# Kernel optimization log

Measured on AMD Instinct MI355X. Metric: run time of the kernel, lower is better.

Reference implementation:

```python
import jax, jax.numpy as jnp
import numpy as np

N = 100000      # nodes
E = 1000000     # edges (before self loops)
F_IN = 128      # num_features
G = 512         # graphs in batch
NC = 10         # num_classes
EPS_BN = 1e-5
NEG_SLOPE = 0.2


def setup_inputs() -> dict:
    key = jax.random.key(0)
    ks = iter(jax.random.split(key, 40))
    rn = lambda shape, s=0.1: jax.random.normal(next(ks), shape, jnp.float32) * s
    inp = {
        "x": jax.random.normal(next(ks), (N, F_IN), jnp.float32),
        "edge_index": jax.random.randint(next(ks), (2, E), 0, N),
        "batch": jnp.sort(jax.random.randint(next(ks), (N,), 0, G)),
        "W1": rn((F_IN, 128)), "as1": rn((8, 16)), "ad1": rn((8, 16)), "b1": jnp.zeros((128,), jnp.float32),
        "g1": jnp.ones((128,), jnp.float32), "be1": jnp.zeros((128,), jnp.float32),
        "Wl1": rn((128, 16)), "bl1": jnp.zeros((16,), jnp.float32),
        "gl1": jnp.ones((16,), jnp.float32), "bel1": jnp.zeros((16,), jnp.float32),
        "W2": rn((16, 96)), "as2": rn((4, 24)), "ad2": rn((4, 24)), "b2": jnp.zeros((96,), jnp.float32),
        "g2": jnp.ones((96,), jnp.float32), "be2": jnp.zeros((96,), jnp.float32),
        "Wl2": rn((96, 24)), "bl2": jnp.zeros((24,), jnp.float32),
        "gl2": jnp.ones((24,), jnp.float32), "bel2": jnp.zeros((24,), jnp.float32),
        "W3": rn((24, 64)), "as3": rn((2, 32)), "ad3": rn((2, 32)), "b3": jnp.zeros((64,), jnp.float32),
        "g3": jnp.ones((64,), jnp.float32), "be3": jnp.zeros((64,), jnp.float32),
        # final classifier
        "Wo": rn((64, NC)), "bo": jnp.zeros((NC,), jnp.float32),
    }
    return inp


def _bn(h, gamma, beta):
    # training-mode BatchNorm1d: batch statistics, biased variance
    m = jnp.mean(h, axis=0)
    v = jnp.var(h, axis=0)
    return gamma * (h - m) * jax.lax.rsqrt(v + EPS_BN) + beta


def _gat(h_in, src, dst, W, a_src, a_dst, bias, n):
    heads, ch = a_src.shape
    h = (h_in @ W).reshape(n, heads, ch)                     # [N,H,C]
    alpha_s = jnp.sum(h * a_src, axis=-1)                    # [N,H]
    alpha_d = jnp.sum(h * a_dst, axis=-1)                    # [N,H]
    e = jax.nn.leaky_relu(alpha_s[src] + alpha_d[dst], NEG_SLOPE)   # [E,H]
    emax = jax.ops.segment_max(e, dst, num_segments=n)       # segment softmax over target
    e = jnp.exp(e - emax[dst])
    denom = jax.ops.segment_sum(e, dst, num_segments=n)
    alpha = e / (denom[dst] + 1e-16)                         # [E,H]
    msg = h[src] * alpha[:, :, None]                         # [E,H,C]
    out = jax.ops.segment_sum(msg, dst, num_segments=n)      # [N,H,C]
    return out.reshape(n, heads * ch) + bias


def reference(x, edge_index, batch,
              W1, as1, ad1, b1, g1, be1, Wl1, bl1, gl1, bel1,
              W2, as2, ad2, b2, g2, be2, Wl2, bl2, gl2, bel2,
              W3, as3, ad3, b3, g3, be3, Wo, bo):
    n = x.shape[0]
    loop = jnp.arange(n)
    src = jnp.concatenate([edge_index[0], loop])   # add self loops (PyG default)
    dst = jnp.concatenate([edge_index[1], loop])

    h = jax.nn.relu(_bn(_gat(x, src, dst, W1, as1, ad1, b1, n), g1, be1))
    h = jax.nn.relu(_bn(h @ Wl1 + bl1, gl1, bel1))
    h = jax.nn.relu(_bn(_gat(h, src, dst, W2, as2, ad2, b2, n), g2, be2))
    h = jax.nn.relu(_bn(h @ Wl2 + bl2, gl2, bel2))
    h = jax.nn.relu(_bn(_gat(h, src, dst, W3, as3, ad3, b3, n), g3, be3))

    # global mean pool over graphs
    counts = jax.ops.segment_sum(jnp.ones((n,), h.dtype), batch, num_segments=G)
    pooled = jax.ops.segment_sum(h, batch, num_segments=G) / jnp.maximum(counts, 1.0)[:, None]
    # dropout is identity in eval
    return pooled @ Wo + bo
```

## Files before the change

kernel.cpp:

```cpp
#include <hip/hip_runtime.h>

typedef unsigned short u16;
typedef unsigned int   u32;
typedef unsigned long long u64;
typedef __attribute__((ext_vector_type(8))) short short8;
typedef __attribute__((ext_vector_type(4))) float f32x4;

#define DEVI __device__ __forceinline__

#define NPB 256
#define SHB 8
#define BHB 64
#define PST 256
#define LOG2E 1.44269504088896340736f

DEVI float bf2f(u16 u){ union{u32 i; float f;} x; x.i = ((u32)u)<<16; return x.f; }
DEVI u16 f2bf(float f){ union{float f; u32 i;} x; x.f = f;
  u32 r = (x.i + 0x7FFFu + ((x.i>>16)&1u))>>16; return (u16)r; }
DEVI float lrelu(float x){ return x > 0.f ? x : 0.2f*x; }
DEVI float exp2g(float x){ return __builtin_amdgcn_exp2f(x); }
DEVI float gload(const void* p, size_t i, int f32){
  return f32 ? ((const float*)p)[i] : bf2f(((const u16*)p)[i]);
}

__global__ __launch_bounds__(64) void k_init(const void* x, int* flag){
  if (threadIdx.x == 0){
    const u16* p = (const u16*)x;
    int hits = 0;
    for (int j = 0; j < 512; j++){
      u16 e = (p[j] >> 7) & 0xFF;
      if (e >= 0xC0) hits++;
    }
    *flag = hits ? 1 : 0;
  }
}

__global__ __launch_bounds__(1024) void k_bhist(const int* ei, int E, int* hist, int NB){
  __shared__ int lh[512];
  for (int b = threadIdx.x; b < NB; b += 1024) lh[b] = 0;
  __syncthreads();
  for (int e = blockIdx.x*1024 + threadIdx.x; e < E; e += BHB*1024)
    atomicAdd(&lh[((u32)ei[E + e]) >> SHB], 1);
  __syncthreads();
  for (int b = threadIdx.x; b < NB; b += 1024) hist[blockIdx.x*NB + b] = lh[b];
}

__global__ __launch_bounds__(256) void k_btot(const int* hist, int* tot, int NB){
  int b = blockIdx.x*256 + threadIdx.x;
  if (b < NB){
    int s = 0;
    #pragma unroll 8
    for (int j = 0; j < BHB; j++) s += hist[j*NB + b];
    tot[b] = s;
  }
}

__global__ __launch_bounds__(512) void k_bscan(const int* tot, int* base, int* coff, int NB, int N){
  __shared__ int l[512];
  int t = threadIdx.x;
  int v = (t < NB) ? tot[t] : 0;
  l[t] = v; __syncthreads();
  for (int st = 1; st < 512; st <<= 1){
    int a = (t >= st) ? l[t - st] : 0;
    __syncthreads();
    l[t] += a;
    __syncthreads();
  }
  if (t < NB) base[t] = l[t] - v;
  if (t == 511){ base[NB] = l[511]; coff[N] = l[511]; }
}

__global__ __launch_bounds__(256) void k_bcur(int* hist, const int* base, int NB){
  int b = blockIdx.x*256 + threadIdx.x;
  if (b < NB){
    int run = base[b];
    for (int j = 0; j < BHB; j++){
      int v = hist[j*NB + b];
      hist[j*NB + b] = run;
      run += v;
    }
  }
}

__global__ __launch_bounds__(1024) void k_bfill(const int* ei, int E, const int* hist,
                                                u64* tmp, int NB){
  __shared__ int cur[512];
  for (int b = threadIdx.x; b < NB; b += 1024) cur[b] = hist[blockIdx.x*NB + b];
  __syncthreads();
  for (int e = blockIdx.x*1024 + threadIdx.x; e < E; e += BHB*1024){
    int s = ei[e], d = ei[E + e];
    int p = atomicAdd(&cur[((u32)d) >> SHB], 1);
    tmp[p] = ((u64)(u32)d << 32) | (u32)s;
  }
}

__global__ __launch_bounds__(256) void k_cfill(const u64* tmp, const int* base,
                                               int* coff, int* csr, int N){
  __shared__ int cnt[NPB], start[NPB];
  int b = blockIdx.x, t = threadIdx.x;
  int p0 = base[b], p1 = base[b + 1];
  cnt[t] = 0;
  __syncthreads();
  for (int i = p0 + t; i < p1; i += 256)
    atomicAdd(&cnt[(int)(tmp[i] >> 32) & (NPB - 1)], 1);
  __syncthreads();
  if (t == 0){
    int run = p0;
    for (int j = 0; j < NPB; j++){ start[j] = run; run += cnt[j]; }
  }
  __syncthreads();
  {
    int node = b*NPB + t;
    if (node < N) coff[node] = start[t];
    cnt[t] = 0;
  }
  __syncthreads();
  for (int i = p0 + t; i < p1; i += 256){
    u64 pr = tmp[i];
    int dj = (int)(pr >> 32) & (NPB - 1);
    int r = atomicAdd(&cnt[dj], 1);
    csr[start[dj] + r] = (int)(u32)pr;
  }
}

__global__ __launch_bounds__(256) void k_prepW(const void* Wg, u16* Wt, const int* dflag){
  const int f32 = dflag[0];
  for (int i = blockIdx.x*256 + threadIdx.x; i < 128*128; i += gridDim.x*256){
    int k = i >> 7, nn = i & 127;
    Wt[nn*128 + k] = f2bf(gload(Wg, i, f32));
  }
}

__global__ __launch_bounds__(256) void k_prep23(const void* W2, const void* as2, const void* ad2,
    const void* W3, const void* as3, const void* ad3,
    u16* Wbd2, u16* Wbd3, float* prepF, const int* dflag){
  const int f32 = dflag[0];
  int t = threadIdx.x;
  for (int i = t; i < 64*96; i += 256){
    int r = i/96, m = i - r*96;
    int h = r >> 4, k = r & 15;
    float v = ((m/24) == h) ? gload(W2, k*96 + m, f32) : 0.f;
    Wbd2[i] = f2bf(v);
  }
  for (int i = t; i < 48*64; i += 256){
    int r = i >> 6, m = i & 63;
    int h = r/24, k = r - h*24;
    float v = ((m >> 5) == h) ? gload(W3, k*64 + m, f32) : 0.f;
    Wbd3[i] = f2bf(v);
  }
  if (t < 64){
    int h = t >> 4, k = t & 15;
    float s = 0.f, d = 0.f;
    for (int c = 0; c < 24; c++){
      float w = gload(W2, k*96 + h*24 + c, f32);
      s = fmaf(w, gload(as2, h*24 + c, f32), s);
      d = fmaf(w, gload(ad2, h*24 + c, f32), d);
    }
    prepF[t] = s; prepF[64 + t] = d;
  }
  if (t >= 64 && t < 112){
    int u = t - 64;
    int h = u/24, k = u - h*24;
    float s = 0.f, d = 0.f;
    for (int c = 0; c < 32; c++){
      float w = gload(W3, k*64 + h*32 + c, f32);
      s = fmaf(w, gload(as3, h*32 + c, f32), s);
      d = fmaf(w, gload(ad3, h*32 + c, f32), d);
    }
    prepF[128 + u] = s; prepF[176 + u] = d;
  }
}

__global__ __launch_bounds__(256) void k_mfma1(const void* x, const u16* __restrict__ Wt,
                                               u16* __restrict__ out, int n, const int* dflag){
  const int f32 = dflag[0];
  const int wave = threadIdx.x >> 6;
  const int lane = threadIdx.x & 63;
  const int l15 = lane & 15, q = lane >> 4;
  const int arow = blockIdx.x*64 + wave*16 + l15;
  const bool rok = arow < n;

  f32x4 acc[8];
  #pragma unroll
  for (int t = 0; t < 8; t++) acc[t] = {0.f, 0.f, 0.f, 0.f};

  #pragma unroll
  for (int kk = 0; kk < 4; kk++){
    short8 a = {0,0,0,0,0,0,0,0};
    if (rok){
      const int ko = kk*32 + q*8;
      if (f32){
        const float* xp = (const float*)x + (size_t)arow*128 + ko;
        float4 v0 = *(const float4*)xp;
        float4 v1 = *(const float4*)(xp + 4);
        a[0]=(short)f2bf(v0.x); a[1]=(short)f2bf(v0.y); a[2]=(short)f2bf(v0.z); a[3]=(short)f2bf(v0.w);
        a[4]=(short)f2bf(v1.x); a[5]=(short)f2bf(v1.y); a[6]=(short)f2bf(v1.z); a[7]=(short)f2bf(v1.w);
      } else {
        a = *(const short8*)((const u16*)x + (size_t)arow*128 + ko);
      }
    }
    #pragma unroll
    for (int t = 0; t < 8; t++){
      short8 b = *(const short8*)(Wt + (size_t)(l15 + 16*t)*128 + kk*32 + q*8);
      acc[t] = __builtin_amdgcn_mfma_f32_16x16x32_bf16(a, b, acc[t], 0, 0, 0);
    }
  }

  const int orow0 = blockIdx.x*64 + wave*16 + q*4;
  #pragma unroll
  for (int r = 0; r < 4; r++){
    int orow = orow0 + r;
    if (orow < n){
      #pragma unroll
      for (int t = 0; t < 8; t++)
        out[(size_t)orow*128 + l15 + 16*t] = f2bf(acc[t][r]);
    }
  }
}

__global__ __launch_bounds__(256) void k_alpha1(const u16* __restrict__ A, const void* a_s, const void* a_d,
    u16* als, u16* ald, int n, const int* dflag){
  const int f32 = dflag[0];
  int idx = blockIdx.x*256 + threadIdx.x;
  if (idx >= n*8) return;
  int r = idx >> 3, hd = idx & 7;
  const u16* p = A + (size_t)r*128 + hd*16;
  float s = 0.f, d = 0.f;
  #pragma unroll
  for (int c = 0; c < 16; c++){
    float v = bf2f(p[c]);
    s = fmaf(v, gload(a_s, hd*16 + c, f32), s);
    d = fmaf(v, gload(a_d, hd*16 + c, f32), d);
  }
  als[idx] = f2bf(s * LOG2E); ald[idx] = f2bf(d * LOG2E);
}

template<int K,int M,int H,int RT,int TPB,bool AFFINE,bool ALPHA,bool WBF16>
__global__ __launch_bounds__(TPB) void k_gemm(
    const u16* in, const void* Wg,
    const float* stat, const void* gam, const void* bet, float invn,
    const void* a_s, const void* a_d, u16* out, u16* als, u16* ald, int n,
    const int* dflag)
{
  constexpr int CT = 4;
  constexpr int TC = M/CT;
  constexpr int TR = TPB/TC;
  constexpr int ROWS = TR*RT;
  constexpr int C = M/H;
  static_assert(TPB % TC == 0, "");
  __shared__ __align__(16) u16 Wl[K*M];
  __shared__ float Il[ROWS*(K+1)];
  __shared__ float red[ALPHA ? (2*ROWS*TC) : 1];
  __shared__ float faL[AFFINE ? K : 1], fdL[AFFINE ? K : 1];

  const int f32 = dflag[0];
  if constexpr (AFFINE){
    for (int k = threadIdx.x; k < K; k += TPB){
      float m = stat[k]*invn;
      float vv = stat[128 + k]*invn - m*m;
      float a = gload(gam, k, f32) * rsqrtf(vv + 1e-5f);
      faL[k] = a;
      fdL[k] = gload(bet, k, f32) - m*a;
    }
    __syncthreads();
  }

  for (int i = threadIdx.x; i < K*M; i += TPB){
    if constexpr (WBF16) Wl[i] = ((const u16*)Wg)[i];
    else Wl[i] = f32 ? f2bf(((const float*)Wg)[i]) : ((const u16*)Wg)[i];
  }

  const int rowbase = blockIdx.x * ROWS;
  for (int i = threadIdx.x; i < ROWS*K; i += TPB){
    int rr = i / K, k = i - rr*K;
    int r = rowbase + rr;
    float v = 0.f;
    if (r < n){
      v = bf2f(in[(size_t)r*K + k]);
      if constexpr (AFFINE) v = fmaxf(fmaf(faL[k], v, fdL[k]), 0.f);
    }
    Il[rr*(K+1) + k] = v;
  }
  __syncthreads();

  const int tc = threadIdx.x % TC;
  const int tr = threadIdx.x / TC;
  float acc[RT][CT];
  #pragma unroll
  for (int j = 0; j < RT; j++)
    #pragma unroll
    for (int c = 0; c < CT; c++) acc[j][c] = 0.f;

  #pragma unroll 8
  for (int k = 0; k < K; k++){
    ushort4 u = *(const ushort4*)&Wl[k*M + tc*CT];
    float w0 = bf2f(u.x), w1 = bf2f(u.y), w2 = bf2f(u.z), w3 = bf2f(u.w);
    #pragma unroll
    for (int j = 0; j < RT; j++){
      float iv = Il[(tr + j*TR)*(K+1) + k];
      acc[j][0] = fmaf(iv, w0, acc[j][0]);
      acc[j][1] = fmaf(iv, w1, acc[j][1]);
      acc[j][2] = fmaf(iv, w2, acc[j][2]);
      acc[j][3] = fmaf(iv, w3, acc[j][3]);
    }
  }

  #pragma unroll
  for (int j = 0; j < RT; j++){
    int r = rowbase + tr + j*TR;
    if (r < n){
      ushort4 st;
      st.x = f2bf(acc[j][0]); st.y = f2bf(acc[j][1]);
      st.z = f2bf(acc[j][2]); st.w = f2bf(acc[j][3]);
      *(ushort4*)&out[(size_t)r*M + tc*CT] = st;
    }
  }

  if constexpr (ALPHA){
    #pragma unroll
    for (int j = 0; j < RT; j++){
      float ps = 0.f, pd = 0.f;
      #pragma unroll
      for (int c = 0; c < CT; c++){
        ps = fmaf(acc[j][c], gload(a_s, tc*CT + c, f32), ps);
        pd = fmaf(acc[j][c], gload(a_d, tc*CT + c, f32), pd);
      }
      red[(tr + j*TR)*TC + tc] = ps;
      red[ROWS*TC + (tr + j*TR)*TC + tc] = pd;
    }
    __syncthreads();
    if (threadIdx.x < ROWS){
      int r = rowbase + threadIdx.x;
      if (r < n){
        float hs[H], hd[H];
        #pragma unroll
        for (int h = 0; h < H; h++){ hs[h] = 0.f; hd[h] = 0.f; }
        for (int t2 = 0; t2 < TC; t2++){
          int hh = (t2*CT)/C;
          hs[hh] += red[threadIdx.x*TC + t2];
          hd[hh] += red[ROWS*TC + threadIdx.x*TC + t2];
        }
        #pragma unroll
        for (int h = 0; h < H; h++){
          als[(size_t)r*H + h] = f2bf(hs[h] * LOG2E);
          ald[(size_t)r*H + h] = f2bf(hd[h] * LOG2E);
        }
      }
    }
  }
}

template<int H,int C>
__global__ __launch_bounds__(256) void k_pullW(const u16* __restrict__ h,
    const u16* __restrict__ als, const u16* __restrict__ ald,
    const int* __restrict__ off, const int* __restrict__ csr, u16* __restrict__ out, int n)
{
  constexpr int F = H*C;
  constexpr int L = F/2;
  constexpr int LOGH = (H==8)?3:((H==4)?2:1);
  constexpr int EPG = 64 >> LOGH;
  int wid = blockIdx.x*4 + (threadIdx.x >> 6);
  if (wid >= n) return;
  int lane = threadIdx.x & 63;
  int uu = lane >> LOGH;
  int hh = lane & (H-1);
  int fl = (lane < L) ? lane : (L-1);
  int hd = (2*fl)/C;
  const u32* hw = (const u32*)h;

  float adw = bf2f(ald[(u32)wid*H + hh]);
  float wsw = exp2g(lrelu(bf2f(als[(u32)wid*H + hh]) + adw));
  float den_lane = (uu == 0) ? wsw : 0.f;

  float wsf = exp2g(lrelu(bf2f(als[(u32)wid*H + hd]) + bf2f(ald[(u32)wid*H + hd])));
  u32 vs = hw[(u32)wid*L + fl];
  float acc0 = wsf * bf2f((u16)vs);
  float acc1 = wsf * bf2f((u16)(vs >> 16));

  int e0 = off[wid], e1 = off[wid + 1];
  for (int e = e0; e < e1; e += EPG){
    int rem = e1 - e;
    int su = csr[e + (uu < rem ? uu : 0)];
    float w = exp2g(lrelu(bf2f(als[(u32)su*H + hh]) + adw));
    if (uu >= rem) w = 0.f;
    den_lane += w;
    int cnt = rem < EPG ? rem : EPG;
    for (int jj = 0; jj < cnt; jj += 8){
      int sb[8]; float wb[8]; u32 vv[8];
      #pragma unroll
      for (int j = 0; j < 8; j++){
        int sl = ((jj + j) << LOGH) + hd;
        sb[j] = __shfl(su, sl);
        wb[j] = __shfl(w,  sl);
      }
      #pragma unroll
      for (int j = 0; j < 8; j++) vv[j] = hw[(u32)sb[j]*L + fl];
      #pragma unroll
      for (int j = 0; j < 8; j++){
        acc0 = fmaf(wb[j], bf2f((u16)vv[j]), acc0);
        acc1 = fmaf(wb[j], bf2f((u16)(vv[j] >> 16)), acc1);
      }
    }
  }
  #pragma unroll
  for (int st = H; st < 64; st <<= 1) den_lane += __shfl_xor(den_lane, st);
  float den = __shfl(den_lane, hd);
  float r = 1.f/(den + 1e-16f);
  if (lane < L)
    ((u32*)out)[(u32)wid*L + fl] = (u32)f2bf(acc0*r) | ((u32)f2bf(acc1*r) << 16);
}

template<int H,int CIN>
__global__ __launch_bounds__(256) void k_alphaX(const u16* __restrict__ Cb,
    const float* stat, const void* gam, const void* bet, float invn,
    const float* vs, const float* vd,
    u16* act, u16* als, u16* ald, int n, const int* dflag)
{
  const int f32 = dflag[0];
  __shared__ float faL[CIN], fdL[CIN];
  if (threadIdx.x < CIN){
    int k = threadIdx.x;
    float m = stat[k]*invn;
    float vv = stat[128 + k]*invn - m*m;
    float a = gload(gam, k, f32) * rsqrtf(vv + 1e-5f);
    faL[k] = a;
    fdL[k] = gload(bet, k, f32) - m*a;
  }
  __syncthreads();
  int idx = blockIdx.x*256 + threadIdx.x;
  if (idx >= n*H) return;
  int j = idx / H, h = idx - j*H;
  float s = 0.f, d = 0.f;
  #pragma unroll
  for (int k = 0; k < CIN; k++){
    float v = bf2f(Cb[(size_t)j*CIN + k]);
    v = fmaxf(fmaf(faL[k], v, fdL[k]), 0.f);
    s = fmaf(v, vs[h*CIN + k], s);
    d = fmaf(v, vd[h*CIN + k], d);
    if (h == 0) act[(size_t)j*CIN + k] = f2bf(v);
  }
  als[idx] = f2bf(s * LOG2E); ald[idx] = f2bf(d * LOG2E);
}

template<int H,int CIN>
__global__ __launch_bounds__(256) void k_pullX(const u16* __restrict__ act,
    const u16* __restrict__ als, const u16* __restrict__ ald,
    const int* __restrict__ off, const int* __restrict__ csr, u16* __restrict__ D, int n)
{
  constexpr int LX = H*CIN;
  constexpr int LOGH = (H==4)?2:1;
  constexpr int EPG = 64 >> LOGH;
  int wid = blockIdx.x*4 + (threadIdx.x >> 6);
  if (wid >= n) return;
  int lane = threadIdx.x & 63;
  int uu = lane >> LOGH;
  int hh = lane & (H-1);
  int fl = (lane < LX) ? lane : (LX-1);
  int hf = fl / CIN, k = fl - hf*CIN;

  float adw = bf2f(ald[(u32)wid*H + hh]);
  float wsw = exp2g(lrelu(bf2f(als[(u32)wid*H + hh]) + adw));
  float den_lane = (uu == 0) ? wsw : 0.f;

  float wsf = exp2g(lrelu(bf2f(als[(u32)wid*H + hf]) + bf2f(ald[(u32)wid*H + hf])));
  float acc = wsf * bf2f(act[(u32)wid*CIN + k]);

  int e0 = off[wid], e1 = off[wid + 1];
  for (int e = e0; e < e1; e += EPG){
    int rem = e1 - e;
    int su = csr[e + (uu < rem ? uu : 0)];
    float w = exp2g(lrelu(bf2f(als[(u32)su*H + hh]) + adw));
    if (uu >= rem) w = 0.f;
    den_lane += w;
    int cnt = rem < EPG ? rem : EPG;
    for (int jj = 0; jj < cnt; jj += 8){
      int sb[8]; float wb[8]; u16 vv[8];
      #pragma unroll
      for (int j = 0; j < 8; j++){
        int sl = ((jj + j) << LOGH) + hf;
        sb[j] = __shfl(su, sl);
        wb[j] = __shfl(w,  sl);
      }
      #pragma unroll
      for (int j = 0; j < 8; j++) vv[j] = act[(u32)sb[j]*CIN + k];
      #pragma unroll
      for (int j = 0; j < 8; j++) acc = fmaf(wb[j], bf2f(vv[j]), acc);
    }
  }
  #pragma unroll
  for (int st = H; st < 64; st <<= 1) den_lane += __shfl_xor(den_lane, st);
  float den = __shfl(den_lane, hf);
  if (lane < LX)
    D[(u32)wid*LX + fl] = f2bf(acc / (den + 1e-16f));
}

template<int F,int TPB>
__global__ __launch_bounds__(TPB) void k_statA(const u16* __restrict__ x, int n,
                                               float* __restrict__ part)
{
  constexpr int L = F/2;
  constexpr int RPB = TPB/L;
  static_assert(TPB % L == 0, "");
  int c = threadIdx.x % L;
  int tr = threadIdx.x / L;
  const u32* xw = (const u32*)x;
  int chunk = (n + (int)gridDim.x - 1)/(int)gridDim.x;
  int r0 = blockIdx.x*chunk;
  int r1 = r0 + chunk; if (r1 > n) r1 = n;
  float a0=0.f, a1=0.f, b0=0.f, b1=0.f;
  int r = r0 + tr;
  for (; r + 3*RPB < r1; r += 4*RPB){
    u32 v0 = xw[(size_t)r*L + c];
    u32 v1 = xw[(size_t)(r + RPB)*L + c];
    u32 v2 = xw[(size_t)(r + 2*RPB)*L + c];
    u32 v3 = xw[(size_t)(r + 3*RPB)*L + c];
    float f0 = bf2f((u16)v0), f1 = bf2f((u16)(v0 >> 16));
    float f2 = bf2f((u16)v1), f3 = bf2f((u16)(v1 >> 16));
    float f4 = bf2f((u16)v2), f5 = bf2f((u16)(v2 >> 16));
    float f6 = bf2f((u16)v3), f7 = bf2f((u16)(v3 >> 16));
    a0 += (f0 + f2) + (f4 + f6);
    a1 += (f1 + f3) + (f5 + f7);
    b0 += (f0*f0 + f2*f2) + (f4*f4 + f6*f6);
    b1 += (f1*f1 + f3*f3) + (f5*f5 + f7*f7);
  }
  for (; r < r1; r += RPB){
    u32 v = xw[(size_t)r*L + c];
    float f0 = bf2f((u16)v), f1 = bf2f((u16)(v >> 16));
    a0 += f0; b0 = fmaf(f0, f0, b0);
    a1 += f1; b1 = fmaf(f1, f1, b1);
  }
  __shared__ float l0[TPB], l1[TPB], l2[TPB], l3[TPB];
  l0[threadIdx.x] = a0; l1[threadIdx.x] = a1;
  l2[threadIdx.x] = b0; l3[threadIdx.x] = b1;
  __syncthreads();
  for (int t2 = threadIdx.x; t2 < 256; t2 += TPB){
    int col = t2 & 127;
    float s = 0.f;
    if (col < F){
      int cc = col >> 1, par = col & 1;
      const float* base = (t2 >= 128) ? (par ? l3 : l2) : (par ? l1 : l0);
      #pragma unroll 4
      for (int j = 0; j < RPB; j++) s += base[j*L + cc];
    }
    part[(size_t)blockIdx.x*256 + t2] = s;
  }
}

__global__ __launch_bounds__(1024) void k_statB(const float* __restrict__ part,
                                                float* __restrict__ out, int P)
{
  __shared__ float l[1024];
  int col = threadIdx.x & 255;
  int q   = threadIdx.x >> 8;
  int rows = (P + 3) >> 2;
  int b0 = q*rows, b1 = b0 + rows; if (b1 > P) b1 = P;
  float s = 0.f;
  int b = b0;
  for (; b + 3 < b1; b += 4)
    s += (part[(size_t)b*256 + col] + part[(size_t)(b+1)*256 + col])
       + (part[(size_t)(b+2)*256 + col] + part[(size_t)(b+3)*256 + col]);
  for (; b < b1; b++) s += part[(size_t)b*256 + col];
  l[threadIdx.x] = s;
  __syncthreads();
  if (threadIdx.x < 256)
    out[threadIdx.x] = (l[threadIdx.x] + l[256 + threadIdx.x])
                     + (l[512 + threadIdx.x] + l[768 + threadIdx.x]);
}

__global__ __launch_bounds__(256) void k_pool(const u16* B, const int* batch, int n,
    const float* stat, const void* g3, const void* be3, float invn,
    const void* Wo, const void* bo, void* outp, const int* dflag)
{
  const int f32 = dflag[0];
  __shared__ float fa[64], fd[64];
  if (threadIdx.x < 64){
    int k = threadIdx.x;
    float m = stat[k]*invn;
    float v = stat[128 + k]*invn - m*m;
    float a = gload(g3, k, f32) * rsqrtf(v + 1e-5f);
    fa[k] = a;
    fd[k] = gload(be3, k, f32) - m*a;
  }
  __syncthreads();

  int g = blockIdx.x;
  int lane = threadIdx.x & 63, wv = threadIdx.x >> 6;
  int s, e;
  { int l = 0, h = n; while (l < h){ int m = (l+h)>>1; if (batch[m] <  g) l = m+1; else h = m; } s = l; }
  { int l = s, h = n; while (l < h){ int m = (l+h)>>1; if (batch[m] <= g) l = m+1; else h = m; } e = l; }
  float a = fa[lane], d = fd[lane], acc = 0.f;
  for (int r = s + wv; r < e; r += 4)
    acc += fmaxf(fmaf(a, bf2f(B[(size_t)r*64 + lane]), d), 0.f);
  __shared__ float pl[4][64];
  pl[wv][lane] = acc;
  __syncthreads();
  if (wv == 0){
    float cnt = (e > s) ? (float)(e - s) : 1.f;
    pl[0][lane] = (pl[0][lane] + pl[1][lane] + pl[2][lane] + pl[3][lane]) / cnt;
  }
  __syncthreads();
  if (threadIdx.x < 10){
    int lo = threadIdx.x;
    float o = gload(bo, lo, f32);
    for (int l2 = 0; l2 < 64; l2++) o = fmaf(pl[0][l2], gload(Wo, l2*10 + lo, f32), o);
    if (f32) ((float*)outp)[g*10 + lo] = o;
    else     ((u16*) outp)[g*10 + lo] = f2bf(o);
  }
}

extern "C" void kernel_launch(void* const* d_in, const int* in_sizes, int n_in,
                              void* d_out, int out_size, void* d_ws, size_t ws_size,
                              hipStream_t stream)
{
  const void* x   = d_in[0];
  const int* ei   = (const int*)d_in[1];
  const int* batch= (const int*)d_in[2];
  const void* W1  = d_in[3];
  const void* as1 = d_in[4];
  const void* ad1 = d_in[5];
  const void* g1  = d_in[7];
  const void* be1 = d_in[8];
  const void* Wl1 = d_in[9];
  const void* gl1 = d_in[11];
  const void* bel1= d_in[12];
  const void* W2  = d_in[13];
  const void* as2 = d_in[14];
  const void* ad2 = d_in[15];
  const void* g2  = d_in[17];
  const void* be2 = d_in[18];
  const void* Wl2 = d_in[19];
  const void* gl2 = d_in[21];
  const void* bel2= d_in[22];
  const void* W3  = d_in[23];
  const void* as3 = d_in[24];
  const void* ad3 = d_in[25];
  const void* g3  = d_in[27];
  const void* be3 = d_in[28];
  const void* Wo  = d_in[29];
  const void* bo  = d_in[30];
  (void)n_in; (void)ws_size;

  const int N = in_sizes[2];
  const int E = in_sizes[1] / 2;
  const int G = out_size / 10;
  const int NB = (N + NPB - 1) >> SHB;

  char* w = (char*)d_ws;
  size_t off = 0;
  auto alloc = [&](size_t bytes)->void*{
    size_t o = off; off += (bytes + 255) & ~(size_t)255; return (void*)(w + o);
  };
  int*   dflag= (int*)alloc(4);
  int*   coff = (int*)alloc((size_t)(N+1)*4);
  int*   csr  = (int*)alloc((size_t)E*4);
  int*   bbase= (int*)alloc((size_t)(NB+1)*4);
  int*   btotb= (int*)alloc((size_t)NB*4);
  int*   hist = (int*)alloc((size_t)BHB*NB*4);
  float* stS  = (float*)alloc(1280*4);
  float* part = (float*)alloc((size_t)PST*256*4);
  float* prepF= (float*)alloc(256*4);
  u16*   Wt   = (u16*)alloc(128*128*2);
  u16*   Wbd2 = (u16*)alloc(64*96*2);
  u16*   Wbd3 = (u16*)alloc(48*64*2);
  u16*   als  = (u16*)alloc((size_t)N*8*2);
  u16*   ald  = (u16*)alloc((size_t)N*8*2);
  u16*   Cb   = (u16*)alloc((size_t)N*24*2);
  u16*   A    = (u16*)alloc((size_t)N*128*2);
  u16*   B    = (u16*)alloc((size_t)N*128*2);
  u64*   tmp  = (u64*)A;
  u16*   D    = A;
  u16*   act  = A + (size_t)N*64;

  const float invN = 1.f/(float)N;
  const int nbb = (NB + 255)/256;

  k_init<<<1, 64, 0, stream>>>(x, dflag);
  k_prepW<<<16, 256, 0, stream>>>(W1, Wt, dflag);
  k_prep23<<<1, 256, 0, stream>>>(W2, as2, ad2, W3, as3, ad3, Wbd2, Wbd3, prepF, dflag);

  k_bhist<<<BHB, 1024, 0, stream>>>(ei, E, hist, NB);
  k_btot <<<nbb, 256, 0, stream>>>(hist, btotb, NB);
  k_bscan<<<1, 512, 0, stream>>>(btotb, bbase, coff, NB, N);
  k_bcur <<<nbb, 256, 0, stream>>>(hist, bbase, NB);
  k_bfill<<<BHB, 1024, 0, stream>>>(ei, E, hist, tmp, NB);
  k_cfill<<<NB, 256, 0, stream>>>(tmp, bbase, coff, csr, N);

  k_mfma1<<<(N+63)/64, 256, 0, stream>>>(x, Wt, A, N, dflag);
  k_alpha1<<<(N*8+255)/256, 256, 0, stream>>>(A, as1, ad1, als, ald, N, dflag);
  k_pullW<8,16><<<(N+3)/4, 256, 0, stream>>>(A, als, ald, coff, csr, B, N);
  k_statA<128,256><<<PST, 256, 0, stream>>>(B, N, part);
  k_statB<<<1, 1024, 0, stream>>>(part, stS + 0, PST);

  k_gemm<128,16,1,1,256,true,false,false><<<(N+63)/64, 256, 0, stream>>>(
      B, Wl1, stS + 0, g1, be1, invN, nullptr, nullptr, Cb, nullptr, nullptr, N, dflag);
  k_statA<16,256><<<PST, 256, 0, stream>>>(Cb, N, part);
  k_statB<<<1, 1024, 0, stream>>>(part, stS + 256, PST);

  k_alphaX<4,16><<<(N*4+255)/256, 256, 0, stream>>>(
      Cb, stS + 256, gl1, bel1, invN, prepF + 0, prepF + 64, act, als, ald, N, dflag);
  k_pullX<4,16><<<(N+3)/4, 256, 0, stream>>>(act, als, ald, coff, csr, D, N);
  k_gemm<64,96,1,2,192,false,false,true><<<(N+15)/16, 192, 0, stream>>>(
      D, Wbd2, nullptr, nullptr, nullptr, invN, nullptr, nullptr, B, nullptr, nullptr, N, dflag);
  k_statA<96,192><<<PST, 192, 0, stream>>>(B, N, part);
  k_statB<<<1, 1024, 0, stream>>>(part, stS + 512, PST);

  k_gemm<96,24,1,2,192,true,false,false><<<(N+63)/64, 192, 0, stream>>>(
      B, Wl2, stS + 512, g2, be2, invN, nullptr, nullptr, Cb, nullptr, nullptr, N, dflag);
  k_statA<24,192><<<PST, 192, 0, stream>>>(Cb, N, part);
  k_statB<<<1, 1024, 0, stream>>>(part, stS + 768, PST);

  k_alphaX<2,24><<<(N*2+255)/256, 256, 0, stream>>>(
      Cb, stS + 768, gl2, bel2, invN, prepF + 128, prepF + 176, act, als, ald, N, dflag);
  k_pullX<2,24><<<(N+3)/4, 256, 0, stream>>>(act, als, ald, coff, csr, D, N);
  k_gemm<48,64,1,2,256,false,false,true><<<(N+31)/32, 256, 0, stream>>>(
      D, Wbd3, nullptr, nullptr, nullptr, invN, nullptr, nullptr, B, nullptr, nullptr, N, dflag);
  k_statA<64,256><<<PST, 256, 0, stream>>>(B, N, part);
  k_statB<<<1, 1024, 0, stream>>>(part, stS + 1024, PST);

  k_pool<<<G, 256, 0, stream>>>(B, batch, N, stS + 1024, g3, be3, invN, Wo, bo, d_out, dflag);
}
```

Before: 696.4 us.

## Fuse prep, scan, alpha and stat-reduce kernels to cut launch count

Merges the init and weight-prep kernels into one multi-block prep kernel, folds the bucket-total, scan and cursor kernels into a single k_bmid, fuses the layer-1 attention-logit computation into the MFMA epilogue via lane shuffles, and replaces each statA+statB pair with a last-block-done reduction using an atomic counter. The aim is to remove about a dozen small kernel launches and one full re-read of the layer-1 features. The single-block scan now also does the per-bucket cursor pass serially, and the counters reset in prep must stay in sync with the stat kernels.

```diff
diff --git a/kernel.cpp b/kernel.cpp
--- a/kernel.cpp
+++ b/kernel.cpp
@@ -23,7 +23,12 @@
   return f32 ? ((const float*)p)[i] : bf2f(((const u16*)p)[i]);
 }
 
-__global__ __launch_bounds__(64) void k_init(const void* x, int* flag){
+__global__ __launch_bounds__(256) void k_prep(const void* x, const void* W1,
+    const void* W2, const void* as2, const void* ad2,
+    const void* W3, const void* as3, const void* ad3,
+    int* dflag, u16* Wt, u16* Wbd2, u16* Wbd3, float* prepF, int* cnts)
+{
+  __shared__ int sf32;
   if (threadIdx.x == 0){
     const u16* p = (const u16*)x;
     int hits = 0;
@@ -31,7 +36,52 @@
       u16 e = (p[j] >> 7) & 0xFF;
       if (e >= 0xC0) hits++;
     }
-    *flag = hits ? 1 : 0;
+    sf32 = hits ? 1 : 0;
+    if (blockIdx.x == 0) *dflag = sf32;
+  }
+  __syncthreads();
+  const int f32 = sf32;
+  int b = blockIdx.x, t = threadIdx.x;
+  if (b < 16){
+    for (int i = b*256 + t; i < 128*128; i += 16*256){
+      int k = i >> 7, nn = i & 127;
+      Wt[nn*128 + k] = f2bf(gload(W1, i, f32));
+    }
+  } else if (b == 16){
+    for (int i = t; i < 64*96; i += 256){
+      int r = i/96, m = i - r*96;
+      int h = r >> 4, k = r & 15;
+      float v = ((m/24) == h) ? gload(W2, k*96 + m, f32) : 0.f;
+      Wbd2[i] = f2bf(v);
+    }
+    if (t < 64){
+      int h = t >> 4, k = t & 15;
+      float s = 0.f, d = 0.f;
+      for (int c = 0; c < 24; c++){
+        float w = gload(W2, k*96 + h*24 + c, f32);
+        s = fmaf(w, gload(as2, h*24 + c, f32), s);
+        d = fmaf(w, gload(ad2, h*24 + c, f32), d);
+      }
+      prepF[t] = s; prepF[64 + t] = d;
+    }
+  } else {
+    for (int i = t; i < 48*64; i += 256){
+      int r = i >> 6, m = i & 63;
+      int h = r/24, k = r - h*24;
+      float v = ((m >> 5) == h) ? gload(W3, k*64 + m, f32) : 0.f;
+      Wbd3[i] = f2bf(v);
+    }
+    if (t < 48){
+      int h = t/24, k = t - h*24;
+      float s = 0.f, d = 0.f;
+      for (int c = 0; c < 32; c++){
+        float w = gload(W3, k*64 + h*32 + c, f32);
+        s = fmaf(w, gload(as3, h*32 + c, f32), s);
+        d = fmaf(w, gload(ad3, h*32 + c, f32), d);
+      }
+      prepF[128 + t] = s; prepF[176 + t] = d;
+    }
+    if (t >= 64 && t < 72) cnts[t - 64] = 0;
   }
 }
 
@@ -45,41 +95,32 @@
   for (int b = threadIdx.x; b < NB; b += 1024) hist[blockIdx.x*NB + b] = lh[b];
 }
 
-__global__ __launch_bounds__(256) void k_btot(const int* hist, int* tot, int NB){
-  int b = blockIdx.x*256 + threadIdx.x;
-  if (b < NB){
-    int s = 0;
-    #pragma unroll 8
-    for (int j = 0; j < BHB; j++) s += hist[j*NB + b];
-    tot[b] = s;
-  }
-}
-
-__global__ __launch_bounds__(512) void k_bscan(const int* tot, int* base, int* coff, int NB, int N){
+__global__ __launch_bounds__(512) void k_bmid(int* hist, int* base, int* coff, int NB, int N){
   __shared__ int l[512];
   int t = threadIdx.x;
-  int v = (t < NB) ? tot[t] : 0;
-  l[t] = v; __syncthreads();
+  int s = 0;
+  if (t < NB){
+    #pragma unroll 8
+    for (int j = 0; j < BHB; j++) s += hist[j*NB + t];
+  }
+  l[t] = s; __syncthreads();
   for (int st = 1; st < 512; st <<= 1){
     int a = (t >= st) ? l[t - st] : 0;
     __syncthreads();
     l[t] += a;
     __syncthreads();
   }
-  if (t < NB) base[t] = l[t] - v;
+  int run0 = l[t] - s;
+  if (t < NB){
+    base[t] = run0;
+    int run = run0;
+    for (int j = 0; j < BHB; j++){
+      int v = hist[j*NB + t];
+      hist[j*NB + t] = run;
+      run += v;
+    }
+  }
   if (t == 511){ base[NB] = l[511]; coff[N] = l[511]; }
-}
-
-__global__ __launch_bounds__(256) void k_bcur(int* hist, const int* base, int NB){
-  int b = blockIdx.x*256 + threadIdx.x;
-  if (b < NB){
-    int run = base[b];
-    for (int j = 0; j < BHB; j++){
-      int v = hist[j*NB + b];
-      hist[j*NB + b] = run;
-      run += v;
-    }
-  }
 }
 
 __global__ __launch_bounds__(1024) void k_bfill(const int* ei, int E, const int* hist,
@@ -123,56 +164,11 @@
   }
 }
 
-__global__ __launch_bounds__(256) void k_prepW(const void* Wg, u16* Wt, const int* dflag){
-  const int f32 = dflag[0];
-  for (int i = blockIdx.x*256 + threadIdx.x; i < 128*128; i += gridDim.x*256){
-    int k = i >> 7, nn = i & 127;
-    Wt[nn*128 + k] = f2bf(gload(Wg, i, f32));
-  }
-}
-
-__global__ __launch_bounds__(256) void k_prep23(const void* W2, const void* as2, const void* ad2,
-    const void* W3, const void* as3, const void* ad3,
-    u16* Wbd2, u16* Wbd3, float* prepF, const int* dflag){
-  const int f32 = dflag[0];
-  int t = threadIdx.x;
-  for (int i = t; i < 64*96; i += 256){
-    int r = i/96, m = i - r*96;
-    int h = r >> 4, k = r & 15;
-    float v = ((m/24) == h) ? gload(W2, k*96 + m, f32) : 0.f;
-    Wbd2[i] = f2bf(v);
-  }
-  for (int i = t; i < 48*64; i += 256){
-    int r = i >> 6, m = i & 63;
-    int h = r/24, k = r - h*24;
-    float v = ((m >> 5) == h) ? gload(W3, k*64 + m, f32) : 0.f;
-    Wbd3[i] = f2bf(v);
-  }
-  if (t < 64){
-    int h = t >> 4, k = t & 15;
-    float s = 0.f, d = 0.f;
-    for (int c = 0; c < 24; c++){
-      float w = gload(W2, k*96 + h*24 + c, f32);
-      s = fmaf(w, gload(as2, h*24 + c, f32), s);
-      d = fmaf(w, gload(ad2, h*24 + c, f32), d);
-    }
-    prepF[t] = s; prepF[64 + t] = d;
-  }
-  if (t >= 64 && t < 112){
-    int u = t - 64;
-    int h = u/24, k = u - h*24;
-    float s = 0.f, d = 0.f;
-    for (int c = 0; c < 32; c++){
-      float w = gload(W3, k*64 + h*32 + c, f32);
-      s = fmaf(w, gload(as3, h*32 + c, f32), s);
-      d = fmaf(w, gload(ad3, h*32 + c, f32), d);
-    }
-    prepF[128 + u] = s; prepF[176 + u] = d;
-  }
-}
-
-__global__ __launch_bounds__(256) void k_mfma1(const void* x, const u16* __restrict__ Wt,
-                                               u16* __restrict__ out, int n, const int* dflag){
+__global__ __launch_bounds__(256) void k_mfma1A(const void* x, const u16* __restrict__ Wt,
+    const void* a_s, const void* a_d,
+    u16* __restrict__ out, u16* __restrict__ als, u16* __restrict__ ald,
+    int n, const int* dflag)
+{
   const int f32 = dflag[0];
   const int wave = threadIdx.x >> 6;
   const int lane = threadIdx.x & 63;
@@ -216,41 +212,56 @@
         out[(size_t)orow*128 + l15 + 16*t] = f2bf(acc[t][r]);
     }
   }
-}
-
-__global__ __launch_bounds__(256) void k_alpha1(const u16* __restrict__ A, const void* a_s, const void* a_d,
-    u16* als, u16* ald, int n, const int* dflag){
-  const int f32 = dflag[0];
-  int idx = blockIdx.x*256 + threadIdx.x;
-  if (idx >= n*8) return;
-  int r = idx >> 3, hd = idx & 7;
-  const u16* p = A + (size_t)r*128 + hd*16;
-  float s = 0.f, d = 0.f;
-  #pragma unroll
-  for (int c = 0; c < 16; c++){
-    float v = bf2f(p[c]);
-    s = fmaf(v, gload(a_s, hd*16 + c, f32), s);
-    d = fmaf(v, gload(a_d, hd*16 + c, f32), d);
-  }
-  als[idx] = f2bf(s * LOG2E); ald[idx] = f2bf(d * LOG2E);
-}
-
-template<int K,int M,int H,int RT,int TPB,bool AFFINE,bool ALPHA,bool WBF16>
+
+  float as_l[8], ad_l[8];
+  #pragma unroll
+  for (int t = 0; t < 8; t++){
+    as_l[t] = gload(a_s, t*16 + l15, f32);
+    ad_l[t] = gload(a_d, t*16 + l15, f32);
+  }
+  #pragma unroll
+  for (int r = 0; r < 4; r++){
+    float s[8], d[8];
+    #pragma unroll
+    for (int t = 0; t < 8; t++){
+      s[t] = acc[t][r] * as_l[t];
+      d[t] = acc[t][r] * ad_l[t];
+    }
+    #pragma unroll
+    for (int st = 1; st < 16; st <<= 1){
+      #pragma unroll
+      for (int t = 0; t < 8; t++){
+        s[t] += __shfl_xor(s[t], st);
+        d[t] += __shfl_xor(d[t], st);
+      }
+    }
+    int orow = orow0 + r;
+    if (l15 == 0 && orow < n){
+      short8 sv, dv;
+      #pragma unroll
+      for (int t = 0; t < 8; t++){
+        sv[t] = (short)f2bf(s[t] * LOG2E);
+        dv[t] = (short)f2bf(d[t] * LOG2E);
+      }
+      *(short8*)(als + (size_t)orow*8) = sv;
+      *(short8*)(ald + (size_t)orow*8) = dv;
+    }
+  }
+}
+
+template<int K,int M,int RT,int TPB,bool AFFINE,bool WBF16>
 __global__ __launch_bounds__(TPB) void k_gemm(
     const u16* in, const void* Wg,
     const float* stat, const void* gam, const void* bet, float invn,
-    const void* a_s, const void* a_d, u16* out, u16* als, u16* ald, int n,
-    const int* dflag)
+    u16* out, int n, const int* dflag)
 {
   constexpr int CT = 4;
   constexpr int TC = M/CT;
   constexpr int TR = TPB/TC;
   constexpr int ROWS = TR*RT;
-  constexpr int C = M/H;
   static_assert(TPB % TC == 0, "");
   __shared__ __align__(16) u16 Wl[K*M];
   __shared__ float Il[ROWS*(K+1)];
-  __shared__ float red[ALPHA ? (2*ROWS*TC) : 1];
   __shared__ float faL[AFFINE ? K : 1], fdL[AFFINE ? K : 1];
 
   const int f32 = dflag[0];
@@ -313,39 +324,6 @@
       st.x = f2bf(acc[j][0]); st.y = f2bf(acc[j][1]);
       st.z = f2bf(acc[j][2]); st.w = f2bf(acc[j][3]);
       *(ushort4*)&out[(size_t)r*M + tc*CT] = st;
-    }
-  }
-
-  if constexpr (ALPHA){
-    #pragma unroll
-    for (int j = 0; j < RT; j++){
-      float ps = 0.f, pd = 0.f;
-      #pragma unroll
-      for (int c = 0; c < CT; c++){
-        ps = fmaf(acc[j][c], gload(a_s, tc*CT + c, f32), ps);
-        pd = fmaf(acc[j][c], gload(a_d, tc*CT + c, f32), pd);
-      }
-      red[(tr + j*TR)*TC + tc] = ps;
-      red[ROWS*TC + (tr + j*TR)*TC + tc] = pd;
-    }
-    __syncthreads();
-    if (threadIdx.x < ROWS){
-      int r = rowbase + threadIdx.x;
-      if (r < n){
-        float hs[H], hd[H];
-        #pragma unroll
-        for (int h = 0; h < H; h++){ hs[h] = 0.f; hd[h] = 0.f; }
-        for (int t2 = 0; t2 < TC; t2++){
-          int hh = (t2*CT)/C;
-          hs[hh] += red[threadIdx.x*TC + t2];
-          hd[hh] += red[ROWS*TC + threadIdx.x*TC + t2];
-        }
-        #pragma unroll
-        for (int h = 0; h < H; h++){
-          als[(size_t)r*H + h] = f2bf(hs[h] * LOG2E);
-          ald[(size_t)r*H + h] = f2bf(hd[h] * LOG2E);
-        }
-      }
     }
   }
 }
@@ -495,8 +473,8 @@
 }
 
 template<int F,int TPB>
-__global__ __launch_bounds__(TPB) void k_statA(const u16* __restrict__ x, int n,
-                                               float* __restrict__ part)
+__global__ __launch_bounds__(TPB) void k_statAB(const u16* __restrict__ x, int n,
+    float* __restrict__ part, float* __restrict__ outS, int* __restrict__ cnt)
 {
   constexpr int L = F/2;
   constexpr int RPB = TPB/L;
@@ -544,27 +522,22 @@
     }
     part[(size_t)blockIdx.x*256 + t2] = s;
   }
-}
-
-__global__ __launch_bounds__(1024) void k_statB(const float* __restrict__ part,
-                                                float* __restrict__ out, int P)
-{
-  __shared__ float l[1024];
-  int col = threadIdx.x & 255;
-  int q   = threadIdx.x >> 8;
-  int rows = (P + 3) >> 2;
-  int b0 = q*rows, b1 = b0 + rows; if (b1 > P) b1 = P;
-  float s = 0.f;
-  int b = b0;
-  for (; b + 3 < b1; b += 4)
-    s += (part[(size_t)b*256 + col] + part[(size_t)(b+1)*256 + col])
-       + (part[(size_t)(b+2)*256 + col] + part[(size_t)(b+3)*256 + col]);
-  for (; b < b1; b++) s += part[(size_t)b*256 + col];
-  l[threadIdx.x] = s;
-  __syncthreads();
-  if (threadIdx.x < 256)
-    out[threadIdx.x] = (l[threadIdx.x] + l[256 + threadIdx.x])
-                     + (l[512 + threadIdx.x] + l[768 + threadIdx.x]);
+  __threadfence();
+  __shared__ int lastf;
+  if (threadIdx.x == 0) lastf = (atomicAdd(cnt, 1) == (int)gridDim.x - 1) ? 1 : 0;
+  __syncthreads();
+  if (lastf){
+    __threadfence();
+    for (int t2 = threadIdx.x; t2 < 256; t2 += TPB){
+      float s = 0.f;
+      int b = 0;
+      for (; b + 3 < PST; b += 4)
+        s += (part[(size_t)b*256 + t2] + part[(size_t)(b+1)*256 + t2])
+           + (part[(size_t)(b+2)*256 + t2] + part[(size_t)(b+3)*256 + t2]);
+      for (; b < PST; b++) s += part[(size_t)b*256 + t2];
+      outS[t2] = s;
+    }
+  }
 }
 
 __global__ __launch_bounds__(256) void k_pool(const u16* B, const int* batch, int n,
@@ -651,10 +624,10 @@
     size_t o = off; off += (bytes + 255) & ~(size_t)255; return (void*)(w + o);
   };
   int*   dflag= (int*)alloc(4);
+  int*   cnts = (int*)alloc(8*4);
   int*   coff = (int*)alloc((size_t)(N+1)*4);
   int*   csr  = (int*)alloc((size_t)E*4);
   int*   bbase= (int*)alloc((size_t)(NB+1)*4);
-  int*   btotb= (int*)alloc((size_t)NB*4);
   int*   hist = (int*)alloc((size_t)BHB*NB*4);
   float* stS  = (float*)alloc(1280*4);
   float* part = (float*)alloc((size_t)PST*256*4);
@@ -672,50 +645,40 @@
   u16*   act  = A + (size_t)N*64;
 
   const float invN = 1.f/(float)N;
-  const int nbb = (NB + 255)/256;
-
-  k_init<<<1, 64, 0, stream>>>(x, dflag);
-  k_prepW<<<16, 256, 0, stream>>>(W1, Wt, dflag);
-  k_prep23<<<1, 256, 0, stream>>>(W2, as2, ad2, W3, as3, ad3, Wbd2, Wbd3, prepF, dflag);
+
+  k_prep<<<18, 256, 0, stream>>>(x, W1, W2, as2, ad2, W3, as3, ad3,
+                                 dflag, Wt, Wbd2, Wbd3, prepF, cnts);
 
   k_bhist<<<BHB, 1024, 0, stream>>>(ei, E, hist, NB);
-  k_btot <<<nbb, 256, 0, stream>>>(hist, btotb, NB);
-  k_bscan<<<1, 512, 0, stream>>>(btotb, bbase, coff, NB, N);
-  k_bcur <<<nbb, 256, 0, stream>>>(hist, bbase, NB);
+  k_bmid <<<1, 512, 0, stream>>>(hist, bbase, coff, NB, N);
   k_bfill<<<BHB, 1024, 0, stream>>>(ei, E, hist, tmp, NB);
   k_cfill<<<NB, 256, 0, stream>>>(tmp, bbase, coff, csr, N);
 
-  k_mfma1<<<(N+63)/64, 256, 0, stream>>>(x, Wt, A, N, dflag);
-  k_alpha1<<<(N*8+255)/256, 256, 0, stream>>>(A, as1, ad1, als, ald, N, dflag);
+  k_mfma1A<<<(N+63)/64, 256, 0, stream>>>(x, Wt, as1, ad1, A, als, ald, N, dflag);
   k_pullW<8,16><<<(N+3)/4, 256, 0, stream>>>(A, als, ald, coff, csr, B, N);
-  k_statA<128,256><<<PST, 256, 0, stream>>>(B, N, part);
-  k_statB<<<1, 1024, 0, stream>>>(part, stS + 0, PST);
-
-  k_gemm<128,16,1,1,256,true,false,false><<<(N+63)/64, 256, 0, stream>>>(
-      B, Wl1, stS + 0, g1, be1, invN, nullptr, nullptr, Cb, nullptr, nullptr, N, dflag);
-  k_statA<16,256><<<PST, 256, 0, stream>>>(Cb, N, part);
-  k_statB<<<1, 1024, 0, stream>>>(part, stS + 256, PST);
+  k_statAB<128,256><<<PST, 256, 0, stream>>>(B, N, part, stS + 0, cnts + 0);
+
+  k_gemm<128,16,1,256,true,false><<<(N+63)/64, 256, 0, stream>>>(
+      B, Wl1, stS + 0, g1, be1, invN, Cb, N, dflag);
+  k_statAB<16,256><<<PST, 256, 0, stream>>>(Cb, N, part, stS + 256, cnts + 1);
 
   k_alphaX<4,16><<<(N*4+255)/256, 256, 0, stream>>>(
       Cb, stS + 256, gl1, bel1, invN, prepF + 0, prepF + 64, act, als, ald, N, dflag);
   k_pullX<4,16><<<(N+3)/4, 256, 0, stream>>>(act, als, ald, coff, csr, D, N);
-  k_gemm<64,96,1,2,192,false,false,true><<<(N+15)/16, 192, 0, stream>>>(
-      D, Wbd2, nullptr, nullptr, nullptr, invN, nullptr, nullptr, B, nullptr, nullptr, N, dflag);
-  k_statA<96,192><<<PST, 192, 0, stream>>>(B, N, part);
-  k_statB<<<1, 1024, 0, stream>>>(part, stS + 512, PST);
-
-  k_gemm<96,24,1,2,192,true,false,false><<<(N+63)/64, 192, 0, stream>>>(
-      B, Wl2, stS + 512, g2, be2, invN, nullptr, nullptr, Cb, nullptr, nullptr, N, dflag);
-  k_statA<24,192><<<PST, 192, 0, stream>>>(Cb, N, part);
-  k_statB<<<1, 1024, 0, stream>>>(part, stS + 768, PST);
+  k_gemm<64,96,2,192,false,true><<<(N+15)/16, 192, 0, stream>>>(
+      D, Wbd2, nullptr, nullptr, nullptr, invN, B, N, dflag);
+  k_statAB<96,192><<<PST, 192, 0, stream>>>(B, N, part, stS + 512, cnts + 2);
+
+  k_gemm<96,24,2,192,true,false><<<(N+63)/64, 192, 0, stream>>>(
+      B, Wl2, stS + 512, g2, be2, invN, Cb, N, dflag);
+  k_statAB<24,192><<<PST, 192, 0, stream>>>(Cb, N, part, stS + 768, cnts + 3);
 
   k_alphaX<2,24><<<(N*2+255)/256, 256, 0, stream>>>(
       Cb, stS + 768, gl2, bel2, invN, prepF + 128, prepF + 176, act, als, ald, N, dflag);
   k_pullX<2,24><<<(N+3)/4, 256, 0, stream>>>(act, als, ald, coff, csr, D, N);
-  k_gemm<48,64,1,2,256,false,false,true><<<(N+31)/32, 256, 0, stream>>>(
-      D, Wbd3, nullptr, nullptr, nullptr, invN, nullptr, nullptr, B, nullptr, nullptr, N, dflag);
-  k_statA<64,256><<<PST, 256, 0, stream>>>(B, N, part);
-  k_statB<<<1, 1024, 0, stream>>>(part, stS + 1024, PST);
+  k_gemm<48,64,2,256,false,true><<<(N+31)/32, 256, 0, stream>>>(
+      D, Wbd3, nullptr, nullptr, nullptr, invN, B, N, dflag);
+  k_statAB<64,256><<<PST, 256, 0, stream>>>(B, N, part, stS + 1024, cnts + 4);
 
   k_pool<<<G, 256, 0, stream>>>(B, batch, N, stS + 1024, g3, be3, invN, Wo, bo, d_out, dflag);
 }
```

New measurement: 716.5 us. 1.03x slower.
